# Kernel optimization log

Hardware: AMD Instinct MI355X
Metric: run time of the kernel (lower is better)

Reference implementation:

```python
import jax, jax.numpy as jnp
import numpy as np

B, N, T_OBS, N_HEAD = 64, 512, 8, 4
IN_FEAT = T_OBS * 2          # 16
OUT_FEAT = IN_FEAT * 4       # 64 (GAT out / MLP in)
HID1, HID2 = 1024, 512
S, NSAMP = 2, 20
OUT_DIM = S * NSAMP          # 40


def setup_inputs() -> dict:
    key = jax.random.key(0)
    ks = jax.random.split(key, 12)
    x = jax.random.normal(ks[0], (B, N, T_OBS, 2), dtype=jnp.float32)
    # binary adjacency-style mask over the dense node-node attention
    mask = (jax.random.uniform(ks[1], (B, 1, N, N)) > 0.1).astype(jnp.float32)
    xav = lambda k, shp, fi, fo: jax.random.uniform(k, shp, jnp.float32, -1.0, 1.0) * (1.414 * np.sqrt(6.0 / (fi + fo)))
    w = xav(ks[2], (N_HEAD, IN_FEAT, OUT_FEAT), IN_FEAT, OUT_FEAT)
    a_src = xav(ks[3], (N_HEAD, OUT_FEAT, 1), OUT_FEAT, 1)
    a_dst = xav(ks[4], (N_HEAD, OUT_FEAT, 1), OUT_FEAT, 1)
    bias = jnp.zeros((OUT_FEAT,), jnp.float32)
    lin = lambda k, fi, fo: jax.random.uniform(k, (fi, fo), jnp.float32, -1.0, 1.0) * np.sqrt(1.0 / fi)
    W1 = lin(ks[5], OUT_FEAT, HID1); b1 = jnp.zeros((HID1,), jnp.float32)
    W2 = lin(ks[6], HID1, HID2);     b2 = jnp.zeros((HID2,), jnp.float32)
    W3 = lin(ks[7], HID2, OUT_DIM);  b3 = jnp.zeros((OUT_DIM,), jnp.float32)
    return {"x": x, "mask": mask, "w": w, "a_src": a_src, "a_dst": a_dst,
            "bias": bias, "W1": W1, "b1": b1, "W2": W2, "b2": b2, "W3": W3, "b3": b3}


def reference(x, mask, w, a_src, a_dst, bias, W1, b1, W2, b2, W3, b3):
    b, n = x.shape[0], x.shape[1]
    node = x.reshape(b, n, -1)                                   # [B,N,16]
    # per-head projection: [B,N,16] x [H,16,64] -> [B,H,N,64]
    h_prime = jnp.einsum('bni,hio->bhno', node, w)
    attn_src = jnp.einsum('bhno,ho->bhn', h_prime, a_src[..., 0])
    attn_dst = jnp.einsum('bhno,ho->bhn', h_prime, a_dst[..., 0])
    attn = attn_src[..., :, None] * attn_dst[..., None, :]       # [B,H,N,N] outer product
    attn = jnp.where(attn >= 0, attn, 0.2 * attn)                # leaky_relu(0.2)
    attn = jax.nn.softmax(attn, axis=-1)
    # dropout is identity in eval mode
    attn = attn * mask
    out = jnp.einsum('bhnm,bhmo->bno', attn, h_prime) + bias     # sum over heads fused
    out = out + h_prime.sum(axis=1)                              # skip connection
    # MLP: activation BEFORE each linear (as in original MLP.forward)
    y = out
    for W, bb in ((W1, b1), (W2, b2), (W3, b3)):
        y = jax.nn.relu(y) @ W + bb
    y = y.reshape(b, n, NSAMP, -1)[..., 0:S]                     # [B,N,20,2]
    return jnp.clip(jax.nn.sigmoid(y), 0.01, 0.99)
```

## Files before the change

kernel.cpp:

```cpp
#include <hip/hip_runtime.h>
#include <math.h>

typedef short bf16x8 __attribute__((ext_vector_type(8)));
typedef float f32x4 __attribute__((ext_vector_type(4)));

#define BB 64
#define NN 512
#define NH 4
#define FI 16
#define FO 64
#define HD1 1024
#define HD2 512
#define ODIM 40

__device__ __forceinline__ unsigned short f2bf(float f) {
    unsigned u = __float_as_uint(f);
    u += 0x7fffu + ((u >> 16) & 1u);
    return (unsigned short)(u >> 16);
}
__device__ __forceinline__ unsigned pack2(float a, float b) {
    return (unsigned)f2bf(a) | ((unsigned)f2bf(b) << 16);
}
__device__ __forceinline__ void gload16(const void* g, void* l) {
    __builtin_amdgcn_global_load_lds(
        (const __attribute__((address_space(1))) unsigned int*)g,
        (__attribute__((address_space(3))) unsigned int*)l,
        16, 0, 0);
}

__global__ void k_wa(const float* __restrict__ w, const float* __restrict__ a_src,
                     const float* __restrict__ a_dst, float* __restrict__ wa)
{
    int t = threadIdx.x;
    int h = t >> 4;
    float s = 0.f, d = 0.f;
    for (int o = 0; o < FO; ++o) {
        float wv = w[t*FO + o];
        s = fmaf(wv, a_src[h*FO + o], s);
        d = fmaf(wv, a_dst[h*FO + o], d);
    }
    wa[t] = s; wa[64 + t] = d;
}

__global__ __launch_bounds__(256) void k_proj2(
    const float* __restrict__ x, const float* __restrict__ w,
    const float* __restrict__ bias, const float* __restrict__ wa,
    short* __restrict__ hpT,
    float* __restrict__ asrc, float* __restrict__ adst,
    float* __restrict__ gat)
{
    __shared__ float xS[64][20];
    __shared__ float gS[NH][64][64];
    int b = blockIdx.y;
    int n0 = blockIdx.x * 64;
    int t = threadIdx.x;
    int h = t >> 6, o = t & 63;
    {
        int n = t >> 2, q = t & 3;
        float4 v = *(const float4*)&x[((size_t)b*NN + n0 + n)*FI + q*4];
        *(float4*)&xS[n][q*4] = v;
    }
    float wreg[16];
#pragma unroll
    for (int i = 0; i < FI; ++i) wreg[i] = w[(h*FI + i)*FO + o];
    __syncthreads();

    short* hb = hpT + (size_t)b * (NH*FO*NN);
    for (int nc = 0; nc < 8; ++nc) {
        float acc[8];
#pragma unroll
        for (int k = 0; k < 8; ++k) {
            int n = nc*8 + k;
            float4 a0 = *(const float4*)&xS[n][0];
            float4 a1 = *(const float4*)&xS[n][4];
            float4 a2 = *(const float4*)&xS[n][8];
            float4 a3 = *(const float4*)&xS[n][12];
            float sA = fmaf(a0.x, wreg[0], fmaf(a0.y, wreg[1], fmaf(a0.z, wreg[2], a0.w*wreg[3])));
            float sB = fmaf(a1.x, wreg[4], fmaf(a1.y, wreg[5], fmaf(a1.z, wreg[6], a1.w*wreg[7])));
            float sC = fmaf(a2.x, wreg[8], fmaf(a2.y, wreg[9], fmaf(a2.z, wreg[10], a2.w*wreg[11])));
            float sD = fmaf(a3.x, wreg[12], fmaf(a3.y, wreg[13], fmaf(a3.z, wreg[14], a3.w*wreg[15])));
            float s = (sA + sB) + (sC + sD);
            acc[k] = s;
            gS[h][n][o] = s;
        }
        uint4 p;
        p.x = pack2(acc[0], acc[1]); p.y = pack2(acc[2], acc[3]);
        p.z = pack2(acc[4], acc[5]); p.w = pack2(acc[6], acc[7]);
        int jt = (n0 >> 5) + (nc >> 2);
        *(uint4*)&hb[(size_t)(jt*256 + h*64 + o)*32 + (nc & 3)*8] = p;
    }
    {
        int n = o;
        float vs = 0.f, vd = 0.f;
#pragma unroll
        for (int i = 0; i < FI; ++i) {
            float xv = xS[n][i];
            vs = fmaf(xv, wa[h*FI + i], vs);
            vd = fmaf(xv, wa[64 + h*FI + i], vd);
        }
        asrc[(size_t)(b*NH + h)*NN + n0 + n] = vs;
        adst[(size_t)(b*NH + h)*NN + n0 + n] = vd;
    }
    __syncthreads();
#pragma unroll
    for (int r = 0; r < 16; ++r) {
        int idx = t + r*256;
        int n = idx >> 6, oo = idx & 63;
        float g = bias[oo] + ((gS[0][n][oo] + gS[1][n][oo]) + (gS[2][n][oo] + gS[3][n][oo]));
        gat[((size_t)b*NN + n0 + n)*FO + oo] = g;
    }
}

__global__ __launch_bounds__(512, 2) void k_attn2(
    const short* __restrict__ hpT, const float* __restrict__ mask,
    const float* __restrict__ asrc, const float* __restrict__ adst,
    float* __restrict__ gat)
{
    __shared__ float dS[NH*NN];
    __shared__ float dmaxS[NH], dminS[NH];
    __shared__ float part[4*4*64*4];
    int b = blockIdx.y;
    int i0blk = blockIdx.x * 64;
    int t = threadIdx.x;
#pragma unroll
    for (int r = 0; r < 4; ++r) {
        int idx = t + r*512;
        dS[idx] = adst[(size_t)b*(NH*NN) + idx];
    }
    __syncthreads();
    int wave = t >> 6, lane = t & 63;
    int wv4 = wave & 3, hh = (wave >> 2) * 2;
    if (wave < 4) {
        float mx = -INFINITY, mn = INFINITY;
        const float* dh = &dS[wave*NN];
#pragma unroll
        for (int q = 0; q < 8; ++q) {
            float v = dh[lane*8 + q];
            mx = fmaxf(mx, v); mn = fminf(mn, v);
        }
#pragma unroll
        for (int off = 1; off < 64; off <<= 1) {
            mx = fmaxf(mx, __shfl_xor(mx, off));
            mn = fminf(mn, __shfl_xor(mn, off));
        }
        if (lane == 0) { dmaxS[wave] = mx; dminS[wave] = mn; }
    }
    __syncthreads();
    int li = lane & 15, kq = lane >> 4;
    int i = i0blk + wv4*16 + li;
    float s[2], m[2], Ssum[2];
#pragma unroll
    for (int h2 = 0; h2 < 2; ++h2) {
        int h = hh + h2;
        s[h2] = asrc[(size_t)(b*NH + h)*NN + i];
        float dm = s[h2] >= 0.f ? dmaxS[h] : dminS[h];
        float l = s[h2] * dm;
        m[h2] = fmaxf(l, 0.2f*l);
        Ssum[h2] = 0.f;
    }
    f32x4 accH[2][4];
#pragma unroll
    for (int h2 = 0; h2 < 2; ++h2)
#pragma unroll
        for (int ot = 0; ot < 4; ++ot) accH[h2][ot] = (f32x4)0.f;

    const float* mrow = &mask[((size_t)b*NN + i)*NN];
    const short* vb = hpT + (size_t)b * (NH*FO*NN);
    float4 mk0 = *(const float4*)&mrow[kq*8];
    float4 mk1 = *(const float4*)&mrow[kq*8 + 4];
    for (int jt = 0; jt < 16; ++jt) {
        float4 c0 = mk0, c1 = mk1;
        if (jt < 15) {
            mk0 = *(const float4*)&mrow[(jt+1)*32 + kq*8];
            mk1 = *(const float4*)&mrow[(jt+1)*32 + kq*8 + 4];
        }
        int j0 = jt*32;
        float mk[8] = {c0.x, c0.y, c0.z, c0.w, c1.x, c1.y, c1.z, c1.w};
#pragma unroll
        for (int h2 = 0; h2 < 2; ++h2) {
            int h = hh + h2;
            float4 d0 = *(const float4*)&dS[h*NN + j0 + kq*8];
            float4 d1 = *(const float4*)&dS[h*NN + j0 + kq*8 + 4];
            float dv[8] = {d0.x,d0.y,d0.z,d0.w,d1.x,d1.y,d1.z,d1.w};
            float u[8];
#pragma unroll
            for (int q = 0; q < 8; ++q) {
                float v = s[h2]*dv[q];
                v = fmaxf(v, 0.2f*v);
                u[q] = __expf(v - m[h2]);
            }
            Ssum[h2] += ((u[0]+u[1]) + (u[2]+u[3])) + ((u[4]+u[5]) + (u[6]+u[7]));
            union { bf16x8 v; unsigned uu[4]; } pf;
#pragma unroll
            for (int q = 0; q < 4; ++q)
                pf.uu[q] = pack2(u[2*q]*mk[2*q], u[2*q+1]*mk[2*q+1]);
            __builtin_amdgcn_s_setprio(1);
#pragma unroll
            for (int ot = 0; ot < 4; ++ot) {
                bf16x8 vf = *(const bf16x8*)&vb[(size_t)(jt*256 + h*64 + ot*16 + li)*32 + kq*8];
                accH[h2][ot] = __builtin_amdgcn_mfma_f32_16x16x32_bf16(pf.v, vf, accH[h2][ot], 0, 0, 0);
            }
            __builtin_amdgcn_s_setprio(0);
        }
    }
#pragma unroll
    for (int h2 = 0; h2 < 2; ++h2) {
        Ssum[h2] += __shfl_xor(Ssum[h2], 16);
        Ssum[h2] += __shfl_xor(Ssum[h2], 32);
    }
    float rinv[2][4];
#pragma unroll
    for (int h2 = 0; h2 < 2; ++h2)
#pragma unroll
        for (int g = 0; g < 4; ++g)
            rinv[h2][g] = 1.0f / __shfl(Ssum[h2], kq*4 + g);
    f32x4 contrib[4];
#pragma unroll
    for (int ot = 0; ot < 4; ++ot)
#pragma unroll
        for (int g = 0; g < 4; ++g)
            contrib[ot][g] = accH[0][ot][g]*rinv[0][g] + accH[1][ot][g]*rinv[1][g];
    if (wave < 4) {
#pragma unroll
        for (int ot = 0; ot < 4; ++ot) {
            float4 v = {contrib[ot][0], contrib[ot][1], contrib[ot][2], contrib[ot][3]};
            *(float4*)&part[((wv4*4 + ot)*64 + lane)*4] = v;
        }
    }
    __syncthreads();
    if (wave >= 4) {
#pragma unroll
        for (int ot = 0; ot < 4; ++ot) {
            float4 p = *(const float4*)&part[((wv4*4 + ot)*64 + lane)*4];
#pragma unroll
            for (int g = 0; g < 4; ++g) {
                int ii = i0blk + wv4*16 + kq*4 + g;
                int oo = ot*16 + li;
                size_t ix = ((size_t)b*NN + ii)*FO + oo;
                float pg = (g == 0) ? p.x : (g == 1) ? p.y : (g == 2) ? p.z : p.w;
                gat[ix] += contrib[ot][g] + pg;
            }
        }
    }
}

__global__ __launch_bounds__(256) void k_conv(
    const float* __restrict__ W1, const float* __restrict__ W2, const float* __restrict__ W3,
    short* __restrict__ w1t, short* __restrict__ w2f, short* __restrict__ w3t)
{
    int idx = blockIdx.x * 256 + threadIdx.x;
    if (idx < HD1*FO) {
        int n = idx >> 6, k = idx & 63;
        w1t[idx] = (short)f2bf(W1[k*HD1 + n]);
    } else if (idx < HD1*FO + HD2*HD1) {
        int i2 = idx - HD1*FO;
        int e = i2 & 7, kqq = (i2 >> 3) & 3, n = (i2 >> 5) & 511, ks = i2 >> 14;
        int k = ks*32 + kqq*8 + e;
        w2f[i2] = (short)f2bf(W2[k*HD2 + n]);
    } else if (idx < HD1*FO + HD2*HD1 + 48*HD2) {
        int i3 = idx - (HD1*FO + HD2*HD1);
        int n = i3 >> 9, k = i3 & 511;
        w3t[i3] = (short)(n < ODIM ? f2bf(W3[k*ODIM + n]) : 0);
    }
}

__global__ __launch_bounds__(256, 2) void k_mlpA(
    const float* __restrict__ gat,
    const short* __restrict__ w1t, const float* __restrict__ b1,
    short* __restrict__ h1g)
{
    __shared__ char a0b[8192];
    int t = threadIdx.x;
    int lane = t & 63, wave = t >> 6;
    int li = lane & 15, kq = lane >> 4;
    int m0 = blockIdx.x * 64;

    {
        int row = t >> 2, c0 = (t & 3) * 16;
        const float4* g = (const float4*)&gat[(size_t)(m0 + row) * FO + c0];
        float4 v0 = g[0], v1 = g[1], v2 = g[2], v3 = g[3];
        uint4 p0, p1;
        p0.x = pack2(fmaxf(v0.x,0.f), fmaxf(v0.y,0.f));
        p0.y = pack2(fmaxf(v0.z,0.f), fmaxf(v0.w,0.f));
        p0.z = pack2(fmaxf(v1.x,0.f), fmaxf(v1.y,0.f));
        p0.w = pack2(fmaxf(v1.z,0.f), fmaxf(v1.w,0.f));
        p1.x = pack2(fmaxf(v2.x,0.f), fmaxf(v2.y,0.f));
        p1.y = pack2(fmaxf(v2.z,0.f), fmaxf(v2.w,0.f));
        p1.z = pack2(fmaxf(v3.x,0.f), fmaxf(v3.y,0.f));
        p1.w = pack2(fmaxf(v3.z,0.f), fmaxf(v3.w,0.f));
        int base = row*128 + c0*2;
        *(uint4*)(a0b + (base ^ ((row&7)<<4)))      = p0;
        *(uint4*)(a0b + ((base+16) ^ ((row&7)<<4))) = p1;
    }
    __syncthreads();

    for (int c = 0; c < 4; ++c) {
        int n0 = wave * 256 + c * 64;
        f32x4 acc[4][4];
#pragma unroll
        for (int mt = 0; mt < 4; ++mt)
#pragma unroll
            for (int nt = 0; nt < 4; ++nt) acc[mt][nt] = (f32x4)0.f;
#pragma unroll
        for (int ks = 0; ks < 2; ++ks) {
            int k0 = ks * 32;
            bf16x8 xf[4];
#pragma unroll
            for (int mt = 0; mt < 4; ++mt) {
                int row = mt * 16 + li;
                int addr = (row * 128 + k0 * 2 + kq * 16) ^ ((row & 7) << 4);
                xf[mt] = *(bf16x8*)(a0b + addr);
            }
#pragma unroll
            for (int nt = 0; nt < 4; ++nt) {
                int col = n0 + nt * 16 + li;
                bf16x8 wf = *(const bf16x8*)(w1t + col * 64 + k0 + kq * 8);
#pragma unroll
                for (int mt = 0; mt < 4; ++mt)
                    acc[mt][nt] = __builtin_amdgcn_mfma_f32_16x16x32_bf16(wf, xf[mt], acc[mt][nt], 0, 0, 0);
            }
        }
#pragma unroll
        for (int mt = 0; mt < 4; ++mt)
#pragma unroll
            for (int nt = 0; nt < 4; ++nt) {
                int m = mt * 16 + li;
                int nb = n0 + nt * 16 + kq * 4;
                float4 bb = *(const float4*)&b1[nb];
                float v0 = fmaxf(acc[mt][nt][0] + bb.x, 0.f);
                float v1 = fmaxf(acc[mt][nt][1] + bb.y, 0.f);
                float v2 = fmaxf(acc[mt][nt][2] + bb.z, 0.f);
                float v3 = fmaxf(acc[mt][nt][3] + bb.w, 0.f);
                uint2 pw; pw.x = pack2(v0, v1); pw.y = pack2(v2, v3);
                *(uint2*)&h1g[(size_t)(m0 + m) * HD1 + nb] = pw;
            }
    }
}

__global__ __launch_bounds__(512, 2) void k_mlpB(
    const short* __restrict__ h1g,
    const short* __restrict__ w2f, const float* __restrict__ b2,
    const short* __restrict__ w3t, const float* __restrict__ b3,
    float* __restrict__ out)
{
    extern __shared__ char smem[];
    int t = threadIdx.x;
    int lane = t & 63, wave = t >> 6;
    int li = lane & 15, kq = lane >> 4;
    int m0 = blockIdx.x * 128;

    auto STAGE = [&](int i, int ks) {
        char* base = smem + i * 8192;
        int row = wave * 16 + (lane >> 2);
        int slotS = (lane & 3) ^ ((row >> 1) & 3);
        const short* src = h1g + (size_t)(m0 + row) * HD1 + ks * 32 + slotS * 8;
        gload16(src, base + wave * 1024);
    };
    const short* wfbase = w2f + ((size_t)(wave*64 + li)*4 + kq)*8;

    f32x4 acc2[8][4];
#pragma unroll
    for (int mt = 0; mt < 8; ++mt)
#pragma unroll
        for (int nt = 0; nt < 4; ++nt) acc2[mt][nt] = (f32x4)0.f;

    bf16x8 wf0[4], wf1[4];
    __builtin_amdgcn_sched_barrier(0);
    STAGE(0, 0);
#pragma unroll
    for (int nt = 0; nt < 4; ++nt) wf0[nt] = *(const bf16x8*)(wfbase + 0*16384 + nt*512);
    __builtin_amdgcn_sched_barrier(0);
    STAGE(1, 1);
#pragma unroll
    for (int nt = 0; nt < 4; ++nt) wf1[nt] = *(const bf16x8*)(wfbase + 1*16384 + nt*512);
    __builtin_amdgcn_sched_barrier(0);

    for (int ks = 0; ks < 32; ++ks) {
        int cur = ks & 1;
        if (ks < 31) { asm volatile("s_waitcnt vmcnt(5)" ::: "memory"); }
        else         { asm volatile("s_waitcnt vmcnt(0)" ::: "memory"); }
        __builtin_amdgcn_sched_barrier(0);
        __builtin_amdgcn_s_barrier();
        __builtin_amdgcn_sched_barrier(0);

        char* base = smem + cur * 8192;
        bf16x8 xf[8];
#pragma unroll
        for (int mt = 0; mt < 8; ++mt) {
            int m = mt * 16 + li;
            int slot = kq ^ ((m >> 1) & 3);
            xf[mt] = *(bf16x8*)(base + m * 64 + slot * 16);
        }
        asm volatile("s_waitcnt lgkmcnt(0)" ::: "memory");
        __builtin_amdgcn_sched_barrier(0);
        __builtin_amdgcn_s_barrier();
        __builtin_amdgcn_sched_barrier(0);

        bf16x8 wfn[4];
        if (ks < 30) {
            STAGE(cur, ks + 2);
#pragma unroll
            for (int nt = 0; nt < 4; ++nt)
                wfn[nt] = *(const bf16x8*)(wfbase + (size_t)(ks+2)*16384 + nt*512);
        }
        __builtin_amdgcn_sched_barrier(0);

        __builtin_amdgcn_s_setprio(1);
#pragma unroll
        for (int nt = 0; nt < 4; ++nt)
#pragma unroll
            for (int mt = 0; mt < 8; ++mt)
                acc2[mt][nt] = __builtin_amdgcn_mfma_f32_16x16x32_bf16(wf0[nt], xf[mt], acc2[mt][nt], 0, 0, 0);
        __builtin_amdgcn_s_setprio(0);
        if (ks < 30) {
#pragma unroll
            for (int nt = 0; nt < 4; ++nt) { wf0[nt] = wf1[nt]; wf1[nt] = wfn[nt]; }
        } else {
#pragma unroll
            for (int nt = 0; nt < 4; ++nt) wf0[nt] = wf1[nt];
        }
    }
    __syncthreads();

#pragma unroll
    for (int mt = 0; mt < 8; ++mt)
#pragma unroll
        for (int nt = 0; nt < 4; ++nt) {
            int m = mt * 16 + li;
            int nb = wave * 64 + nt * 16 + kq * 4;
            float4 bb = *(const float4*)&b2[nb];
            float v0 = fmaxf(acc2[mt][nt][0] + bb.x, 0.f);
            float v1 = fmaxf(acc2[mt][nt][1] + bb.y, 0.f);
            float v2 = fmaxf(acc2[mt][nt][2] + bb.z, 0.f);
            float v3 = fmaxf(acc2[mt][nt][3] + bb.w, 0.f);
            uint2 pw; pw.x = pack2(v0, v1); pw.y = pack2(v2, v3);
            int addr = (m * 1024 + nb * 2) ^ ((m & 7) << 4);
            *(uint2*)(smem + addr) = pw;
        }
    __syncthreads();

    f32x4 acc3[3];
#pragma unroll
    for (int nt = 0; nt < 3; ++nt) acc3[nt] = (f32x4)0.f;
#pragma unroll
    for (int ks = 0; ks < 16; ++ks) {
        int k0 = ks * 32;
        int m = wave * 16 + li;
        int addr = (m * 1024 + k0 * 2 + kq * 16) ^ ((m & 7) << 4);
        bf16x8 xfr = *(bf16x8*)(smem + addr);
#pragma unroll
        for (int nt = 0; nt < 3; ++nt) {
            int col = nt * 16 + li;
            bf16x8 wfr = *(const bf16x8*)(w3t + col * 512 + k0 + kq * 8);
            acc3[nt] = __builtin_amdgcn_mfma_f32_16x16x32_bf16(wfr, xfr, acc3[nt], 0, 0, 0);
        }
    }
#pragma unroll
    for (int nt = 0; nt < 3; ++nt)
#pragma unroll
        for (int g = 0; g < 4; ++g) {
            int n = nt * 16 + kq * 4 + g;
            if (n < ODIM) {
                int m = wave * 16 + li;
                float s = acc3[nt][g] + b3[n];
                s = 1.f / (1.f + __expf(-s));
                s = fminf(fmaxf(s, 0.01f), 0.99f);
                out[(size_t)(m0 + m) * ODIM + n] = s;
            }
        }
}

extern "C" void kernel_launch(void* const* d_in, const int* in_sizes, int n_in,
                              void* d_out, int out_size, void* d_ws, size_t ws_size,
                              hipStream_t stream)
{
    const float* x     = (const float*)d_in[0];
    const float* mask  = (const float*)d_in[1];
    const float* w     = (const float*)d_in[2];
    const float* a_src = (const float*)d_in[3];
    const float* a_dst = (const float*)d_in[4];
    const float* bias  = (const float*)d_in[5];
    const float* W1    = (const float*)d_in[6];
    const float* b1    = (const float*)d_in[7];
    const float* W2    = (const float*)d_in[8];
    const float* b2    = (const float*)d_in[9];
    const float* W3    = (const float*)d_in[10];
    const float* b3    = (const float*)d_in[11];
    float* out = (float*)d_out;

    char* p = (char*)d_ws;
    short* h1g = (short*)p;
    short* hpT = (short*)p;  p += (size_t)BB*NH*FO*NN*2;
    float* asrc = (float*)p; p += (size_t)BB*NH*NN*4;
    float* adst = (float*)p; p += (size_t)BB*NH*NN*4;
    p = (char*)d_ws + (size_t)BB*NN*HD1*2;
    float* gat  = (float*)p; p += (size_t)BB*NN*FO*4;
    short* w1t  = (short*)p; p += (size_t)HD1*FO*2;
    short* w2f  = (short*)p; p += (size_t)HD2*HD1*2;
    short* w3t  = (short*)p; p += (size_t)48*HD2*2;
    float* wa   = (float*)p; p += 128*4;

    k_wa   <<<1, 64, 0, stream>>>(w, a_src, a_dst, wa);
    k_conv <<<(HD1*FO + HD2*HD1 + 48*HD2)/256, 256, 0, stream>>>(W1, W2, W3, w1t, w2f, w3t);
    k_proj2<<<dim3(NN/64, BB), 256, 0, stream>>>(x, w, bias, wa, hpT, asrc, adst, gat);
    k_attn2<<<dim3(NN/64, BB), 512, 0, stream>>>(hpT, mask, asrc, adst, gat);
    k_mlpA <<<BB*NN/64, 256, 0, stream>>>(gat, w1t, b1, h1g);
    k_mlpB <<<BB*NN/128, 512, 131072, stream>>>(h1g, w2f, b2, w3t, b3, out);
}
```

Baseline: 161.4 us.

## Pack float attention mask into bitmask before attention kernel

Adds a pre-pass kernel that turns the dense float mask into one bit per entry (64 bytes per row). The attention kernel then loads each row's bits once and selects the softmax numerators by bit test instead of streaming float mask values inside its main loop. The goal is to take the large mask stream out of the compute-heavy attention kernel and shrink its register and load pressure. In exchange, the full float mask must still be read once by the new kernel, which adds a launch and a serial bandwidth-bound step. The change also assumes the mask is binary, treating any nonzero value as 1.

```diff
diff --git a/kernel.cpp b/kernel.cpp
--- a/kernel.cpp
+++ b/kernel.cpp
@@ -40,6 +40,33 @@
         d = fmaf(wv, a_dst[h*FO + o], d);
     }
     wa[t] = s; wa[64 + t] = d;
+}
+
+__global__ __launch_bounds__(256) void k_pack(
+    const float* __restrict__ mask, unsigned char* __restrict__ mbits)
+{
+    __shared__ unsigned char lb[4][64];
+    int t = threadIdx.x;
+    int r = t >> 6, l = t & 63;
+    size_t R = (size_t)blockIdx.x * 4 + r;
+    const float4* src = (const float4*)(mask + R*NN + l*8);
+    float4 a = src[0], bq = src[1];
+    unsigned byte = 0;
+    byte |= (a.x  != 0.f) ? 1u   : 0u;
+    byte |= (a.y  != 0.f) ? 2u   : 0u;
+    byte |= (a.z  != 0.f) ? 4u   : 0u;
+    byte |= (a.w  != 0.f) ? 8u   : 0u;
+    byte |= (bq.x != 0.f) ? 16u  : 0u;
+    byte |= (bq.y != 0.f) ? 32u  : 0u;
+    byte |= (bq.z != 0.f) ? 64u  : 0u;
+    byte |= (bq.w != 0.f) ? 128u : 0u;
+    lb[r][(l & 3)*16 + (l >> 2)] = (unsigned char)byte;
+    __syncthreads();
+    if (t < 16) {
+        int rr = t >> 2, seg = t & 3;
+        uint4 v = *(uint4*)&lb[rr][seg*16];
+        *(uint4*)&mbits[((size_t)blockIdx.x*4 + rr)*64 + seg*16] = v;
+    }
 }
 
 __global__ __launch_bounds__(256) void k_proj2(
@@ -112,7 +139,7 @@
 }
 
 __global__ __launch_bounds__(512, 2) void k_attn2(
-    const short* __restrict__ hpT, const float* __restrict__ mask,
+    const short* __restrict__ hpT, const unsigned char* __restrict__ mbits,
     const float* __restrict__ asrc, const float* __restrict__ adst,
     float* __restrict__ gat)
 {
@@ -164,18 +191,16 @@
 #pragma unroll
         for (int ot = 0; ot < 4; ++ot) accH[h2][ot] = (f32x4)0.f;
 
-    const float* mrow = &mask[((size_t)b*NN + i)*NN];
+    unsigned mwarr[4];
+    {
+        uint4 mv = *(const uint4*)(mbits + ((size_t)(b*NN + i))*64 + kq*16);
+        mwarr[0] = mv.x; mwarr[1] = mv.y; mwarr[2] = mv.z; mwarr[3] = mv.w;
+    }
     const short* vb = hpT + (size_t)b * (NH*FO*NN);
-    float4 mk0 = *(const float4*)&mrow[kq*8];
-    float4 mk1 = *(const float4*)&mrow[kq*8 + 4];
+#pragma unroll
     for (int jt = 0; jt < 16; ++jt) {
-        float4 c0 = mk0, c1 = mk1;
-        if (jt < 15) {
-            mk0 = *(const float4*)&mrow[(jt+1)*32 + kq*8];
-            mk1 = *(const float4*)&mrow[(jt+1)*32 + kq*8 + 4];
-        }
+        unsigned mbyte = (mwarr[jt >> 2] >> ((jt & 3) * 8)) & 0xffu;
         int j0 = jt*32;
-        float mk[8] = {c0.x, c0.y, c0.z, c0.w, c1.x, c1.y, c1.z, c1.w};
 #pragma unroll
         for (int h2 = 0; h2 < 2; ++h2) {
             int h = hh + h2;
@@ -190,10 +215,14 @@
                 u[q] = __expf(v - m[h2]);
             }
             Ssum[h2] += ((u[0]+u[1]) + (u[2]+u[3])) + ((u[4]+u[5]) + (u[6]+u[7]));
+            float mu[8];
+#pragma unroll
+            for (int q = 0; q < 8; ++q)
+                mu[q] = ((mbyte >> q) & 1u) ? u[q] : 0.f;
             union { bf16x8 v; unsigned uu[4]; } pf;
 #pragma unroll
             for (int q = 0; q < 4; ++q)
-                pf.uu[q] = pack2(u[2*q]*mk[2*q], u[2*q+1]*mk[2*q+1]);
+                pf.uu[q] = pack2(mu[2*q], mu[2*q+1]);
             __builtin_amdgcn_s_setprio(1);
 #pragma unroll
             for (int ot = 0; ot < 4; ++ot) {
@@ -499,11 +528,13 @@
     short* w2f  = (short*)p; p += (size_t)HD2*HD1*2;
     short* w3t  = (short*)p; p += (size_t)48*HD2*2;
     float* wa   = (float*)p; p += 128*4;
+    unsigned char* mbits = (unsigned char*)p; p += (size_t)BB*NN*64;
 
     k_wa   <<<1, 64, 0, stream>>>(w, a_src, a_dst, wa);
+    k_pack <<<BB*NN/4, 256, 0, stream>>>(mask, mbits);
     k_conv <<<(HD1*FO + HD2*HD1 + 48*HD2)/256, 256, 0, stream>>>(W1, W2, W3, w1t, w2f, w3t);
     k_proj2<<<dim3(NN/64, BB), 256, 0, stream>>>(x, w, bias, wa, hpT, asrc, adst, gat);
-    k_attn2<<<dim3(NN/64, BB), 512, 0, stream>>>(hpT, mask, asrc, adst, gat);
+    k_attn2<<<dim3(NN/64, BB), 512, 0, stream>>>(hpT, mbits, asrc, adst, gat);
     k_mlpA <<<BB*NN/64, 256, 0, stream>>>(gat, w1t, b1, h1g);
     k_mlpB <<<BB*NN/128, 512, 131072, stream>>>(h1g, w2f, b2, w3t, b3, out);
 }
```

Result: no change. 160.4 us (median of 2 runs) (-0.6%).
